# Kernel tuning notes

Measured on AMD Instinct MI355X. Metric: run time of the kernel, lower is better.

The kernel has to match this reference:

```python
import jax, jax.numpy as jnp
import numpy as np
import math

B, L, D, H, DFF = 2, 2048, 1024, 16, 4096

def _mha(xq, xkv, Wq, bq, Wk, bk, Wv, bv, Wo, bo, mask, h):
    # xq: [B,Lq,D], xkv: [B,Lk,D], mask: [B,1,Lq,Lk] bool
    b, lq, d = xq.shape
    dk = d // h
    q = (xq @ Wq + bq).reshape(b, lq, h, dk).transpose(0, 2, 1, 3)        # [B,h,Lq,dk]
    k = (xkv @ Wk + bk).reshape(b, -1, h, dk).transpose(0, 2, 1, 3)       # [B,h,Lk,dk]
    v = (xkv @ Wv + bv).reshape(b, -1, h, dk).transpose(0, 2, 1, 3)       # [B,h,Lk,dk]
    scores = jnp.einsum('bhqd,bhkd->bhqk', q, k) / jnp.sqrt(jnp.float32(dk))
    scores = jnp.where(mask, scores, jnp.float32(-1e9))                   # masked_fill(mask==0, -1e9)
    prob = jax.nn.softmax(scores, axis=-1)
    out = jnp.einsum('bhqk,bhkd->bhqd', prob, v)
    out = out.transpose(0, 2, 1, 3).reshape(b, lq, d)
    return out @ Wo + bo

def setup_inputs() -> dict:
    key = jax.random.key(0)
    ks = jax.random.split(key, 16)
    s = 0.02
    inp = {
        'tgt': jax.random.normal(ks[0], (B, L, D), jnp.float32),
        'encoder_out': jax.random.normal(ks[1], (B, L, D), jnp.float32),
        'tgt_mask': jnp.broadcast_to(jnp.tril(jnp.ones((L, L), bool)), (B, 1, L, L)),
        'src_tgt_mask': jnp.ones((B, 1, L, L), bool),
    }
    names = ['sWq','sWk','sWv','sWo','cWq','cWk','cWv','cWo']
    for i, n in enumerate(names):
        inp[n] = s * jax.random.normal(ks[2 + i], (D, D), jnp.float32)
        inp['sb' + n[2] if n[0] == 's' else 'cb' + n[2]] = jnp.zeros((D,), jnp.float32)
    inp['W1'] = s * jax.random.normal(ks[10], (D, DFF), jnp.float32)
    inp['b1'] = jnp.zeros((DFF,), jnp.float32)
    inp['W2'] = s * jax.random.normal(ks[11], (DFF, D), jnp.float32)
    inp['b2'] = jnp.zeros((D,), jnp.float32)
    return inp

def reference(tgt, encoder_out, tgt_mask, src_tgt_mask,
              sWq, sbq, sWk, sbk, sWv, sbv, sWo, sbo,
              cWq, cbq, cWk, cbk, cWv, cbv, cWo, cbo,
              W1, b1, W2, b2):
    # residual 1: masked self-attention (no norm)
    x = tgt + _mha(tgt, tgt, sWq, sbq, sWk, sbk, sWv, sbv, sWo, sbo, tgt_mask, H)
    # residual 2: cross-attention over encoder_out
    x = x + _mha(x, encoder_out, cWq, cbq, cWk, cbk, cWv, cbv, cWo, cbo, src_tgt_mask, H)
    # residual 3: position-wise FFN with ReLU
    x = x + (jax.nn.relu(x @ W1 + b1) @ W2 + b2)
    return x
```

## Files before the change

kernel.cpp:

```cpp
#include <hip/hip_runtime.h>

typedef unsigned short u16;
typedef unsigned int u32;
typedef __attribute__((ext_vector_type(8))) short short8;
typedef __attribute__((ext_vector_type(8))) __bf16 bf16x8;
typedef __attribute__((ext_vector_type(4))) float f32x4;
typedef __attribute__((ext_vector_type(4))) u16 u16x4;
typedef __attribute__((ext_vector_type(2))) u32 u32x2;

#define GLD16(gp, lp) __builtin_amdgcn_global_load_lds( \
    (const __attribute__((address_space(1))) unsigned int*)(gp), \
    (__attribute__((address_space(3))) unsigned int*)(lp), 16, 0, 0)

#if defined(__has_builtin) && __has_builtin(__builtin_amdgcn_exp2f)
#define EXP2(x) __builtin_amdgcn_exp2f(x)
#else
static __device__ __forceinline__ float exp2_asm(float x){
  float r; asm("v_exp_f32 %0, %1" : "=v"(r) : "v"(x)); return r;
}
#define EXP2(x) exp2_asm(x)
#endif

__device__ __forceinline__ float bf2f(u16 u){
  unsigned x = ((unsigned)u) << 16; float f; __builtin_memcpy(&f, &x, 4); return f;
}
__device__ __forceinline__ u16 f2bf(float f){
  unsigned x; __builtin_memcpy(&x, &f, 4);
  x += 0x7fffu + ((x >> 16) & 1u);
  return (u16)(x >> 16);
}
__device__ __forceinline__ u32 pkhi(float lo, float hi){
  u32 a, b; __builtin_memcpy(&a, &lo, 4); __builtin_memcpy(&b, &hi, 4);
  return __builtin_amdgcn_perm(b, a, 0x07060302u);
}
__device__ __forceinline__ f32x4 mfma_bf16(short8 a, short8 b, f32x4 c){
  return __builtin_amdgcn_mfma_f32_16x16x32_bf16(
      __builtin_bit_cast(bf16x8, a), __builtin_bit_cast(bf16x8, b), c, 0, 0, 0);
}

__global__ __launch_bounds__(256) void k_conv(const float* __restrict__ s, u16* __restrict__ d, int n){
  int i4 = (blockIdx.x * 256 + threadIdx.x) * 4;
  if (i4 < n){
    float4 v = *(const float4*)(s + i4);
    u16x4 o; o.x = f2bf(v.x); o.y = f2bf(v.y); o.z = f2bf(v.z); o.w = f2bf(v.w);
    *(u16x4*)(d + i4) = o;
  }
}

__global__ __launch_bounds__(256) void k_transpose(const float* __restrict__ s, u16* __restrict__ d, int K, int N){
  __shared__ float t[32][33];
  int bx = blockIdx.x * 32, by = blockIdx.y * 32;
  int x = threadIdx.x & 31, y = threadIdx.x >> 5;
  #pragma unroll
  for (int i = 0; i < 4; i++)
    t[y + i*8][x] = s[(size_t)(by + y + i*8) * N + bx + x];
  __syncthreads();
  #pragma unroll
  for (int i = 0; i < 4; i++)
    d[(size_t)(bx + y + i*8) * K + by + x] = f2bf(t[x][y + i*8]);
}

struct TP8 { const float* s[8]; u16* d[8]; };
__global__ __launch_bounds__(256) void k_transpose8(TP8 p){
  __shared__ float t[32][33];
  const float* s = p.s[blockIdx.z];
  u16* d = p.d[blockIdx.z];
  int bx = blockIdx.x * 32, by = blockIdx.y * 32;
  int x = threadIdx.x & 31, y = threadIdx.x >> 5;
  #pragma unroll
  for (int i = 0; i < 4; i++)
    t[y + i*8][x] = s[(size_t)(by + y + i*8) * 1024 + bx + x];
  __syncthreads();
  #pragma unroll
  for (int i = 0; i < 4; i++)
    d[(size_t)(bx + y + i*8) * 1024 + by + x] = f2bf(t[x][y + i*8]);
}

__global__ __launch_bounds__(256) void k_packbias(
    const float* __restrict__ sbq, const float* __restrict__ sbk,
    const float* __restrict__ sbv, const float* __restrict__ cbk,
    const float* __restrict__ cbv, float* __restrict__ pbS,
    float* __restrict__ pbC){
  int i = blockIdx.x * 256 + threadIdx.x;
  if (i < 3072) pbS[i] = (i < 1024) ? sbq[i] : (i < 2048 ? sbk[i-1024] : sbv[i-2048]);
  if (i < 2048) pbC[i] = (i < 1024) ? cbk[i] : cbv[i-1024];
}

template<int EPI, int BM, int BN, int KU>
__global__ __launch_bounds__(256, 2) void k_gemm_bt(
    const u16* __restrict__ A, const u16* __restrict__ BT,
    const float* __restrict__ bias, const float* __restrict__ resid,
    float* __restrict__ outF, u16* __restrict__ outB,
    int M, int N, int K, int vt_start, u16* __restrict__ Vt){
  constexpr int MI = BM / 32, NI = BN / 32;
  __shared__ u16 As[2*KU][BM*32];
  __shared__ u16 Bs[2*KU][BN*32];
  int tid = threadIdx.x, wave = tid >> 6, lane = tid & 63;
  int bm = blockIdx.x * BM, bn = blockIdx.y * BN;
  int wm = (wave & 1) * (BM/2), wn = (wave >> 1) * (BN/2);
  int l15 = lane & 15, quad = lane >> 4;

  f32x4 z = {0.f, 0.f, 0.f, 0.f};
  f32x4 acc[MI][NI];
  #pragma unroll
  for (int a = 0; a < MI; a++)
    #pragma unroll
    for (int b = 0; b < NI; b++) acc[a][b] = z;

  int sr = wave*16 + (lane >> 2);
  int sc = (lane & 3) * 8;
  const u16* Ag = A  + (size_t)(bm + sr) * K + sc;
  const u16* Bg = BT + (size_t)(bn + sr) * K + sc;
  int NKP = (K >> 5) / KU;

  #pragma unroll
  for (int u = 0; u < KU; u++){
    #pragma unroll
    for (int i = 0; i < BM/64; i++)
      GLD16(Ag + (size_t)(i*64)*K + u*32, &As[u][(wave*16 + i*64) * 32]);
    #pragma unroll
    for (int i = 0; i < BN/64; i++)
      GLD16(Bg + (size_t)(i*64)*K + u*32, &Bs[u][(wave*16 + i*64) * 32]);
  }

  for (int kt = 0; kt < NKP; kt++){
    __syncthreads();
    int cur = (kt & 1) * KU;
    if (kt + 1 < NKP){
      int nb = cur ^ KU;
      #pragma unroll
      for (int u = 0; u < KU; u++){
        int k0 = ((kt + 1) * KU + u) * 32;
        #pragma unroll
        for (int i = 0; i < BM/64; i++)
          GLD16(Ag + (size_t)(i*64)*K + k0, &As[nb+u][(wave*16 + i*64) * 32]);
        #pragma unroll
        for (int i = 0; i < BN/64; i++)
          GLD16(Bg + (size_t)(i*64)*K + k0, &Bs[nb+u][(wave*16 + i*64) * 32]);
      }
    }
    #pragma unroll
    for (int u = 0; u < KU; u++){
      short8 af[MI], bf[NI];
      #pragma unroll
      for (int mi = 0; mi < MI; mi++)
        af[mi] = *(const short8*)&As[cur+u][(wm + mi*16 + l15)*32 + quad*8];
      #pragma unroll
      for (int ni = 0; ni < NI; ni++)
        bf[ni] = *(const short8*)&Bs[cur+u][(wn + ni*16 + l15)*32 + quad*8];
      #pragma unroll
      for (int mi = 0; mi < MI; mi++)
        #pragma unroll
        for (int ni = 0; ni < NI; ni++)
          acc[mi][ni] = mfma_bf16(af[mi], bf[ni], acc[mi][ni]);
    }
  }

  #pragma unroll
  for (int mi = 0; mi < MI; mi++){
    #pragma unroll
    for (int ni = 0; ni < NI; ni++){
      int col = bn + wn + ni*16 + l15;
      float bv = bias[col];
      if (EPI == 0 && col >= vt_start){
        int vc = col - vt_start;
        int hh = vc >> 6, dd = vc & 63;
        int row0 = bm + wm + mi*16 + quad*4;
        int bb = row0 >> 11, ll = row0 & 2047;
        u16x4 vv;
        #pragma unroll
        for (int r = 0; r < 4; r++) vv[r] = f2bf(acc[mi][ni][r] + bv);
        *(u16x4*)&Vt[(((size_t)bb*16 + hh)*64 + dd)*2048 + ll] = vv;
      } else {
        #pragma unroll
        for (int r = 0; r < 4; r++){
          int row = bm + wm + mi*16 + quad*4 + r;
          float v = acc[mi][ni][r] + bv;
          if (EPI == 1) v = v > 0.f ? v : 0.f;
          size_t idx = (size_t)row * N + col;
          if (EPI >= 2) v += resid[idx];
          if (EPI == 2 || EPI == 3) outF[idx] = v;
          if (EPI != 3) outB[idx] = f2bf(v);
        }
      }
    }
  }
}

template<bool CAUSAL>
__global__ __launch_bounds__(256, 2) void k_flash(
    const u16* __restrict__ Q, int ldq,
    const u16* __restrict__ Kg, int ldk,
    const u16* __restrict__ Vt,
    u16* __restrict__ O, int ldo){
  __shared__ u16 Ks[128*64];
  __shared__ u16 Vs[64*128];
  __shared__ u16 Ps[128*128];
  int tid = threadIdx.x, wave = tid >> 6, lane = tid & 63;
  int l15 = lane & 15, quad = lane >> 4;
  int bx = blockIdx.x;
  int qt = CAUSAL ? ((bx & 1) ? (15 - (bx >> 1)) : (bx >> 1)) : bx;
  int bh = blockIdx.y;
  int b = bh >> 4, h = bh & 15;
  size_t bL = (size_t)b * 2048;
  const u16* qp = Q  + (bL + qt*128) * (size_t)ldq + h*64;
  const u16* kp = Kg + bL * (size_t)ldk + h*64;
  const u16* vtp = Vt + (size_t)bh * 64 * 2048;
  int wm = wave * 32;

  const float QSCALE = 0.125f * 1.44269504088896f;
  short8 qf[2][2];
  #pragma unroll
  for (int mi = 0; mi < 2; mi++)
    #pragma unroll
    for (int ks = 0; ks < 2; ks++){
      short8 t = *(const short8*)(qp + (size_t)(wm + mi*16 + l15)*ldq + ks*32 + quad*8);
      #pragma unroll
      for (int j = 0; j < 8; j++)
        t[j] = (short)f2bf(bf2f((u16)t[j]) * QSCALE);
      qf[mi][ks] = t;
    }

  f32x4 z = {0.f, 0.f, 0.f, 0.f};
  f32x4 o[2][4];
  float mrow[2], lrow[2];
  #pragma unroll
  for (int mi = 0; mi < 2; mi++){ mrow[mi] = -3.0e38f; lrow[mi] = 0.f; }
  #pragma unroll
  for (int mi = 0; mi < 2; mi++)
    #pragma unroll
    for (int nd = 0; nd < 4; nd++) o[mi][nd] = z;

  int nkt = CAUSAL ? (qt + 1) : 16;
  for (int kt = 0; kt < nkt; kt++){
    int cg = ((lane & 7) ^ ((lane >> 3) & 7)) * 8;
    #pragma unroll
    for (int i = 0; i < 4; i++){
      int r = i*32 + wave*8 + (lane >> 3);
      GLD16(kp + (size_t)(kt*128 + r) * ldk + cg, &Ks[(i*32 + wave*8) * 64]);
    }
    #pragma unroll
    for (int i = 0; i < 4; i++){
      int d0 = i*16 + wave*4;
      int d = d0 + (lane >> 4);
      int j = lane & 15;
      int chunk = (j & 8) | ((j ^ (d & 7)) & 7);
      GLD16(vtp + (size_t)d*2048 + kt*128 + chunk*8, &Vs[d0*128]);
    }
    __syncthreads();

    f32x4 s[2][8];
    #pragma unroll
    for (int mi = 0; mi < 2; mi++)
      #pragma unroll
      for (int nk = 0; nk < 8; nk++) s[mi][nk] = z;
    #pragma unroll
    for (int ks = 0; ks < 2; ks++){
      short8 kf[8];
      #pragma unroll
      for (int nk = 0; nk < 8; nk++){
        int row = nk*16 + l15;
        kf[nk] = *(const short8*)&Ks[row*64 + (((ks*4 + quad) ^ (row & 7)))*8];
      }
      #pragma unroll
      for (int mi = 0; mi < 2; mi++)
        #pragma unroll
        for (int nk = 0; nk < 8; nk++)
          s[mi][nk] = mfma_bf16(kf[nk], qf[mi][ks], s[mi][nk]);
    }

    if (CAUSAL && kt == qt){
      #pragma unroll
      for (int mi = 0; mi < 2; mi++){
        int q = wm + mi*16 + l15;
        #pragma unroll
        for (int nk = 0; nk < 8; nk++)
          #pragma unroll
          for (int r = 0; r < 4; r++){
            int key = nk*16 + quad*4 + r;
            if (key > q) s[mi][nk][r] = -1e30f;
          }
      }
    }

    #pragma unroll
    for (int mi = 0; mi < 2; mi++){
      float mx = s[mi][0][0];
      #pragma unroll
      for (int nk = 0; nk < 8; nk++)
        #pragma unroll
        for (int r = 0; r < 4; r++) mx = fmaxf(mx, s[mi][nk][r]);
      mx = fmaxf(mx, __shfl_xor(mx, 16));
      mx = fmaxf(mx, __shfl_xor(mx, 32));
      float mnew = fmaxf(mrow[mi], mx);
      float alpha = EXP2(mrow[mi] - mnew);
      mrow[mi] = mnew;
      float ls = 0.f;
      #pragma unroll
      for (int nk = 0; nk < 8; nk++)
        #pragma unroll
        for (int r = 0; r < 4; r++){
          float p = EXP2(s[mi][nk][r] - mnew);
          s[mi][nk][r] = p;
          ls += p;
        }
      ls += __shfl_xor(ls, 16);
      ls += __shfl_xor(ls, 32);
      lrow[mi] = lrow[mi] * alpha + ls;
      #pragma unroll
      for (int r = 0; r < 4; r++){
        float ar = __shfl(alpha, quad*20 + r);
        #pragma unroll
        for (int nd = 0; nd < 4; nd++) o[mi][nd][r] *= ar;
      }
    }

    #pragma unroll
    for (int mi = 0; mi < 2; mi++){
      int row = wm + mi*16 + l15;
      #pragma unroll
      for (int nk = 0; nk < 8; nk++){
        u32x2 pw;
        pw.x = pkhi(s[mi][nk][0], s[mi][nk][1]);
        pw.y = pkhi(s[mi][nk][2], s[mi][nk][3]);
        int c = nk*4 + quad;
        int phys = c ^ (row & 14);
        *(u32x2*)&Ps[row*128 + phys*4] = pw;
      }
    }

    #pragma unroll
    for (int kc = 0; kc < 4; kc++){
      short8 vf[4], pf[2];
      #pragma unroll
      for (int nd = 0; nd < 4; nd++){
        int d = nd*16 + l15;
        int cc = kc*4 + quad;
        int phys = (cc & 8) | ((cc ^ (d & 7)) & 7);
        vf[nd] = *(const short8*)&Vs[d*128 + phys*8];
      }
      #pragma unroll
      for (int mi = 0; mi < 2; mi++){
        int row = wm + mi*16 + l15;
        int c = kc*8 + quad*2;
        int phys = c ^ (row & 14);
        pf[mi] = *(const short8*)&Ps[row*128 + phys*4];
      }
      #pragma unroll
      for (int mi = 0; mi < 2; mi++)
        #pragma unroll
        for (int nd = 0; nd < 4; nd++)
          o[mi][nd] = mfma_bf16(pf[mi], vf[nd], o[mi][nd]);
    }
    __syncthreads();
  }

  u16* op = O + (bL + qt*128) * (size_t)ldo + h*64;
  #pragma unroll
  for (int mi = 0; mi < 2; mi++){
    float invl = 1.f / lrow[mi];
    #pragma unroll
    for (int r = 0; r < 4; r++){
      float ir = __shfl(invl, quad*20 + r);
      #pragma unroll
      for (int nd = 0; nd < 4; nd++)
        op[(size_t)(wm + mi*16 + quad*4 + r)*ldo + nd*16 + l15] = f2bf(o[mi][nd][r] * ir);
    }
  }
}

extern "C" void kernel_launch(void* const* d_in, const int* in_sizes, int n_in,
                              void* d_out, int out_size, void* d_ws, size_t ws_size,
                              hipStream_t stream){
  (void)in_sizes; (void)n_in; (void)out_size; (void)ws_size;
  const float* tgt = (const float*)d_in[0];
  const float* enc = (const float*)d_in[1];
  const float* sWq = (const float*)d_in[4];  const float* sbq = (const float*)d_in[5];
  const float* sWk = (const float*)d_in[6];  const float* sbk = (const float*)d_in[7];
  const float* sWv = (const float*)d_in[8];  const float* sbv = (const float*)d_in[9];
  const float* sWo = (const float*)d_in[10]; const float* sbo = (const float*)d_in[11];
  const float* cWq = (const float*)d_in[12]; const float* cbq = (const float*)d_in[13];
  const float* cWk = (const float*)d_in[14]; const float* cbk = (const float*)d_in[15];
  const float* cWv = (const float*)d_in[16]; const float* cbv = (const float*)d_in[17];
  const float* cWo = (const float*)d_in[18]; const float* cbo = (const float*)d_in[19];
  const float* W1  = (const float*)d_in[20]; const float* b1  = (const float*)d_in[21];
  const float* W2  = (const float*)d_in[22]; const float* b2  = (const float*)d_in[23];
  float* out = (float*)d_out;

  const int M = 4096;
  const int NEVER = 1 << 30;
  char* w = (char*)d_ws;
  auto alloc = [&](size_t bytes)->void*{ void* p = w; w += (bytes + 255) & ~(size_t)255; return p; };
  u16* tb    = (u16*)alloc((size_t)M*1024*2);
  u16* eb    = (u16*)alloc((size_t)M*1024*2);
  u16* qkv   = (u16*)alloc((size_t)M*3072*2);
  u16* ao    = (u16*)alloc((size_t)M*1024*2);
  u16* xb    = (u16*)alloc((size_t)M*1024*2);
  float* x1f = (float*)alloc((size_t)M*1024*4);
  u16* hbuf  = (u16*)alloc((size_t)M*4096*2);
  u16* VtS   = (u16*)alloc((size_t)32*64*2048*2);
  u16* VtC   = (u16*)alloc((size_t)32*64*2048*2);
  u16* sQKVT = (u16*)alloc((size_t)3072*1024*2);
  u16* sWoT  = (u16*)alloc((size_t)1024*1024*2);
  u16* cWqT  = (u16*)alloc((size_t)1024*1024*2);
  u16* cKVT  = (u16*)alloc((size_t)2048*1024*2);
  u16* cWoT  = (u16*)alloc((size_t)1024*1024*2);
  u16* W1T   = (u16*)alloc((size_t)4096*1024*2);
  u16* W2T   = (u16*)alloc((size_t)1024*4096*2);
  float* pbS = (float*)alloc(3072*4);
  float* pbC = (float*)alloc(2048*4);
  u16* cq  = tb;
  u16* ckv = qkv;

  k_conv<<<dim3(4096), 256, 0, stream>>>(tgt, tb, M*1024);
  k_conv<<<dim3(4096), 256, 0, stream>>>(enc, eb, M*1024);
  TP8 tp;
  tp.s[0]=sWq; tp.s[1]=sWk; tp.s[2]=sWv; tp.s[3]=sWo;
  tp.s[4]=cWq; tp.s[5]=cWk; tp.s[6]=cWv; tp.s[7]=cWo;
  tp.d[0]=sQKVT; tp.d[1]=sQKVT+1024*1024; tp.d[2]=sQKVT+2048*1024; tp.d[3]=sWoT;
  tp.d[4]=cWqT; tp.d[5]=cKVT; tp.d[6]=cKVT+1024*1024; tp.d[7]=cWoT;
  k_transpose8<<<dim3(32,32,8), 256, 0, stream>>>(tp);
  k_transpose<<<dim3(128,32), 256, 0, stream>>>(W1, W1T, 1024, 4096);
  k_transpose<<<dim3(32,128), 256, 0, stream>>>(W2, W2T, 4096, 1024);
  k_packbias<<<dim3(12), 256, 0, stream>>>(sbq, sbk, sbv, cbk, cbv, pbS, pbC);

  k_gemm_bt<0,128,128,1><<<dim3(32,24), 256, 0, stream>>>(tb, sQKVT, pbS, nullptr, nullptr, qkv, M, 3072, 1024, 2048, VtS);
  k_flash<true><<<dim3(16,32), 256, 0, stream>>>(qkv, 3072, qkv+1024, 3072, VtS, ao, 1024);
  k_gemm_bt<2,64,64,2><<<dim3(64,16), 256, 0, stream>>>(ao, sWoT, sbo, tgt, x1f, xb, M, 1024, 1024, NEVER, nullptr);

  k_gemm_bt<0,64,64,2><<<dim3(64,16), 256, 0, stream>>>(xb, cWqT, cbq, nullptr, nullptr, cq, M, 1024, 1024, NEVER, nullptr);
  k_gemm_bt<0,128,128,1><<<dim3(32,16), 256, 0, stream>>>(eb, cKVT, pbC, nullptr, nullptr, ckv, M, 2048, 1024, 1024, VtC);
  k_flash<false><<<dim3(16,32), 256, 0, stream>>>(cq, 1024, ckv, 2048, VtC, ao, 1024);
  k_gemm_bt<2,64,64,2><<<dim3(64,16), 256, 0, stream>>>(ao, cWoT, cbo, x1f, x1f, xb, M, 1024, 1024, NEVER, nullptr);

  k_gemm_bt<1,128,128,1><<<dim3(32,32), 256, 0, stream>>>(xb, W1T, b1, nullptr, nullptr, hbuf, M, 4096, 1024, NEVER, nullptr);
  k_gemm_bt<3,64,64,2><<<dim3(64,16), 256, 0, stream>>>(hbuf, W2T, b2, x1f, out, nullptr, M, 1024, 4096, NEVER, nullptr);
}
```

Baseline: 543.4 us.

## Shrink flash tiles to 64x64 and double-buffer K/V loads in LDS

The flash attention kernel now handles 64 query rows per block with 64-key tiles instead of 128x128. K and V tiles are double-buffered in LDS, so the next tile's global-to-LDS load is issued while the current tile is computed. The smaller tiles double the grid, cut LDS use and registers, and raise the launch bound to 4 blocks per CU for more occupancy and better causal load balance. The cost is half the MFMA work per wave for each K/V load, more loop iterations and more barriers.

```diff
diff --git a/kernel.cpp b/kernel.cpp
--- a/kernel.cpp
+++ b/kernel.cpp
@@ -188,184 +188,166 @@
 }
 
 template<bool CAUSAL>
-__global__ __launch_bounds__(256, 2) void k_flash(
+__global__ __launch_bounds__(256, 4) void k_flash(
     const u16* __restrict__ Q, int ldq,
     const u16* __restrict__ Kg, int ldk,
     const u16* __restrict__ Vt,
     u16* __restrict__ O, int ldo){
-  __shared__ u16 Ks[128*64];
-  __shared__ u16 Vs[64*128];
-  __shared__ u16 Ps[128*128];
+  __shared__ u16 Ks[2][64*64];
+  __shared__ u16 Vs[2][64*64];
+  __shared__ u16 Ps[64*64];
   int tid = threadIdx.x, wave = tid >> 6, lane = tid & 63;
   int l15 = lane & 15, quad = lane >> 4;
   int bx = blockIdx.x;
-  int qt = CAUSAL ? ((bx & 1) ? (15 - (bx >> 1)) : (bx >> 1)) : bx;
+  int qt = CAUSAL ? ((bx & 1) ? (31 - (bx >> 1)) : (bx >> 1)) : bx;
   int bh = blockIdx.y;
   int b = bh >> 4, h = bh & 15;
   size_t bL = (size_t)b * 2048;
-  const u16* qp = Q  + (bL + qt*128) * (size_t)ldq + h*64;
+  const u16* qp = Q  + (bL + qt*64) * (size_t)ldq + h*64;
   const u16* kp = Kg + bL * (size_t)ldk + h*64;
   const u16* vtp = Vt + (size_t)bh * 64 * 2048;
-  int wm = wave * 32;
+  int wm = wave * 16;
 
   const float QSCALE = 0.125f * 1.44269504088896f;
-  short8 qf[2][2];
-  #pragma unroll
-  for (int mi = 0; mi < 2; mi++)
+  short8 qf[2];
+  #pragma unroll
+  for (int ks = 0; ks < 2; ks++){
+    short8 t = *(const short8*)(qp + (size_t)(wm + l15)*ldq + ks*32 + quad*8);
+    #pragma unroll
+    for (int j = 0; j < 8; j++)
+      t[j] = (short)f2bf(bf2f((u16)t[j]) * QSCALE);
+    qf[ks] = t;
+  }
+
+  f32x4 z = {0.f, 0.f, 0.f, 0.f};
+  f32x4 o[4];
+  float mrow = -3.0e38f, lrow = 0.f;
+  #pragma unroll
+  for (int nd = 0; nd < 4; nd++) o[nd] = z;
+
+  int srow = wave*8 + (lane >> 3);
+  int scol = ((lane & 7) ^ ((lane >> 3) & 7)) * 8;
+
+  int nkt = CAUSAL ? (qt + 1) : 32;
+  #pragma unroll
+  for (int i = 0; i < 2; i++)
+    GLD16(kp + (size_t)(i*32 + srow) * ldk + scol, &Ks[0][(i*32 + wave*8) * 64]);
+  #pragma unroll
+  for (int i = 0; i < 2; i++)
+    GLD16(vtp + (size_t)(i*32 + srow) * 2048 + scol, &Vs[0][(i*32 + wave*8) * 64]);
+
+  for (int kt = 0; kt < nkt; kt++){
+    __syncthreads();
+    int cur = kt & 1;
+    if (kt + 1 < nkt){
+      int nb = cur ^ 1;
+      #pragma unroll
+      for (int i = 0; i < 2; i++)
+        GLD16(kp + (size_t)((kt+1)*64 + i*32 + srow) * ldk + scol, &Ks[nb][(i*32 + wave*8) * 64]);
+      #pragma unroll
+      for (int i = 0; i < 2; i++)
+        GLD16(vtp + (size_t)(i*32 + srow) * 2048 + (kt+1)*64 + scol, &Vs[nb][(i*32 + wave*8) * 64]);
+    }
+
+    f32x4 s[4];
+    #pragma unroll
+    for (int nk = 0; nk < 4; nk++) s[nk] = z;
     #pragma unroll
     for (int ks = 0; ks < 2; ks++){
-      short8 t = *(const short8*)(qp + (size_t)(wm + mi*16 + l15)*ldq + ks*32 + quad*8);
-      #pragma unroll
-      for (int j = 0; j < 8; j++)
-        t[j] = (short)f2bf(bf2f((u16)t[j]) * QSCALE);
-      qf[mi][ks] = t;
-    }
-
-  f32x4 z = {0.f, 0.f, 0.f, 0.f};
-  f32x4 o[2][4];
-  float mrow[2], lrow[2];
-  #pragma unroll
-  for (int mi = 0; mi < 2; mi++){ mrow[mi] = -3.0e38f; lrow[mi] = 0.f; }
-  #pragma unroll
-  for (int mi = 0; mi < 2; mi++)
-    #pragma unroll
-    for (int nd = 0; nd < 4; nd++) o[mi][nd] = z;
-
-  int nkt = CAUSAL ? (qt + 1) : 16;
-  for (int kt = 0; kt < nkt; kt++){
-    int cg = ((lane & 7) ^ ((lane >> 3) & 7)) * 8;
-    #pragma unroll
-    for (int i = 0; i < 4; i++){
-      int r = i*32 + wave*8 + (lane >> 3);
-      GLD16(kp + (size_t)(kt*128 + r) * ldk + cg, &Ks[(i*32 + wave*8) * 64]);
-    }
-    #pragma unroll
-    for (int i = 0; i < 4; i++){
-      int d0 = i*16 + wave*4;
-      int d = d0 + (lane >> 4);
-      int j = lane & 15;
-      int chunk = (j & 8) | ((j ^ (d & 7)) & 7);
-      GLD16(vtp + (size_t)d*2048 + kt*128 + chunk*8, &Vs[d0*128]);
-    }
-    __syncthreads();
-
-    f32x4 s[2][8];
-    #pragma unroll
-    for (int mi = 0; mi < 2; mi++)
-      #pragma unroll
-      for (int nk = 0; nk < 8; nk++) s[mi][nk] = z;
-    #pragma unroll
-    for (int ks = 0; ks < 2; ks++){
-      short8 kf[8];
-      #pragma unroll
-      for (int nk = 0; nk < 8; nk++){
+      short8 kf[4];
+      #pragma unroll
+      for (int nk = 0; nk < 4; nk++){
         int row = nk*16 + l15;
-        kf[nk] = *(const short8*)&Ks[row*64 + (((ks*4 + quad) ^ (row & 7)))*8];
-      }
-      #pragma unroll
-      for (int mi = 0; mi < 2; mi++)
-        #pragma unroll
-        for (int nk = 0; nk < 8; nk++)
-          s[mi][nk] = mfma_bf16(kf[nk], qf[mi][ks], s[mi][nk]);
+        kf[nk] = *(const short8*)&Ks[cur][row*64 + (((ks*4 + quad) ^ (row & 7)))*8];
+      }
+      #pragma unroll
+      for (int nk = 0; nk < 4; nk++)
+        s[nk] = mfma_bf16(kf[nk], qf[ks], s[nk]);
     }
 
     if (CAUSAL && kt == qt){
-      #pragma unroll
-      for (int mi = 0; mi < 2; mi++){
-        int q = wm + mi*16 + l15;
-        #pragma unroll
-        for (int nk = 0; nk < 8; nk++)
-          #pragma unroll
-          for (int r = 0; r < 4; r++){
-            int key = nk*16 + quad*4 + r;
-            if (key > q) s[mi][nk][r] = -1e30f;
-          }
-      }
-    }
-
-    #pragma unroll
-    for (int mi = 0; mi < 2; mi++){
-      float mx = s[mi][0][0];
-      #pragma unroll
-      for (int nk = 0; nk < 8; nk++)
-        #pragma unroll
-        for (int r = 0; r < 4; r++) mx = fmaxf(mx, s[mi][nk][r]);
+      int q = wm + l15;
+      #pragma unroll
+      for (int nk = 0; nk < 4; nk++)
+        #pragma unroll
+        for (int r = 0; r < 4; r++){
+          int key = nk*16 + quad*4 + r;
+          if (key > q) s[nk][r] = -1e30f;
+        }
+    }
+
+    {
+      float mx = s[0][0];
+      #pragma unroll
+      for (int nk = 0; nk < 4; nk++)
+        #pragma unroll
+        for (int r = 0; r < 4; r++) mx = fmaxf(mx, s[nk][r]);
       mx = fmaxf(mx, __shfl_xor(mx, 16));
       mx = fmaxf(mx, __shfl_xor(mx, 32));
-      float mnew = fmaxf(mrow[mi], mx);
-      float alpha = EXP2(mrow[mi] - mnew);
-      mrow[mi] = mnew;
+      float mnew = fmaxf(mrow, mx);
+      float alpha = EXP2(mrow - mnew);
+      mrow = mnew;
       float ls = 0.f;
       #pragma unroll
-      for (int nk = 0; nk < 8; nk++)
+      for (int nk = 0; nk < 4; nk++)
         #pragma unroll
         for (int r = 0; r < 4; r++){
-          float p = EXP2(s[mi][nk][r] - mnew);
-          s[mi][nk][r] = p;
+          float p = EXP2(s[nk][r] - mnew);
+          s[nk][r] = p;
           ls += p;
         }
       ls += __shfl_xor(ls, 16);
       ls += __shfl_xor(ls, 32);
-      lrow[mi] = lrow[mi] * alpha + ls;
+      lrow = lrow * alpha + ls;
       #pragma unroll
       for (int r = 0; r < 4; r++){
         float ar = __shfl(alpha, quad*20 + r);
         #pragma unroll
-        for (int nd = 0; nd < 4; nd++) o[mi][nd][r] *= ar;
-      }
-    }
-
-    #pragma unroll
-    for (int mi = 0; mi < 2; mi++){
-      int row = wm + mi*16 + l15;
-      #pragma unroll
-      for (int nk = 0; nk < 8; nk++){
+        for (int nd = 0; nd < 4; nd++) o[nd][r] *= ar;
+      }
+    }
+
+    {
+      int row = wm + l15;
+      #pragma unroll
+      for (int nk = 0; nk < 4; nk++){
         u32x2 pw;
-        pw.x = pkhi(s[mi][nk][0], s[mi][nk][1]);
-        pw.y = pkhi(s[mi][nk][2], s[mi][nk][3]);
+        pw.x = pkhi(s[nk][0], s[nk][1]);
+        pw.y = pkhi(s[nk][2], s[nk][3]);
         int c = nk*4 + quad;
         int phys = c ^ (row & 14);
-        *(u32x2*)&Ps[row*128 + phys*4] = pw;
-      }
-    }
-
-    #pragma unroll
-    for (int kc = 0; kc < 4; kc++){
-      short8 vf[4], pf[2];
+        *(u32x2*)&Ps[row*64 + phys*4] = pw;
+      }
+    }
+
+    #pragma unroll
+    for (int kc = 0; kc < 2; kc++){
+      short8 vf[4];
       #pragma unroll
       for (int nd = 0; nd < 4; nd++){
         int d = nd*16 + l15;
         int cc = kc*4 + quad;
-        int phys = (cc & 8) | ((cc ^ (d & 7)) & 7);
-        vf[nd] = *(const short8*)&Vs[d*128 + phys*8];
-      }
-      #pragma unroll
-      for (int mi = 0; mi < 2; mi++){
-        int row = wm + mi*16 + l15;
-        int c = kc*8 + quad*2;
-        int phys = c ^ (row & 14);
-        pf[mi] = *(const short8*)&Ps[row*128 + phys*4];
-      }
-      #pragma unroll
-      for (int mi = 0; mi < 2; mi++)
-        #pragma unroll
-        for (int nd = 0; nd < 4; nd++)
-          o[mi][nd] = mfma_bf16(pf[mi], vf[nd], o[mi][nd]);
-    }
-    __syncthreads();
-  }
-
-  u16* op = O + (bL + qt*128) * (size_t)ldo + h*64;
-  #pragma unroll
-  for (int mi = 0; mi < 2; mi++){
-    float invl = 1.f / lrow[mi];
-    #pragma unroll
-    for (int r = 0; r < 4; r++){
-      float ir = __shfl(invl, quad*20 + r);
+        int phys = cc ^ (d & 7);
+        vf[nd] = *(const short8*)&Vs[cur][d*64 + phys*8];
+      }
+      int row = wm + l15;
+      int pc = kc*8 + quad*2;
+      int pphys = pc ^ (row & 14);
+      short8 pf = *(const short8*)&Ps[row*64 + pphys*4];
       #pragma unroll
       for (int nd = 0; nd < 4; nd++)
-        op[(size_t)(wm + mi*16 + quad*4 + r)*ldo + nd*16 + l15] = f2bf(o[mi][nd][r] * ir);
-    }
+        o[nd] = mfma_bf16(pf, vf[nd], o[nd]);
+    }
+  }
+
+  u16* op = O + (bL + qt*64) * (size_t)ldo + h*64;
+  float invl = 1.f / lrow;
+  #pragma unroll
+  for (int r = 0; r < 4; r++){
+    float ir = __shfl(invl, quad*20 + r);
+    #pragma unroll
+    for (int nd = 0; nd < 4; nd++)
+      op[(size_t)(wm + quad*4 + r)*ldo + nd*16 + l15] = f2bf(o[nd][r] * ir);
   }
 }
 
@@ -425,12 +407,12 @@
   k_packbias<<<dim3(12), 256, 0, stream>>>(sbq, sbk, sbv, cbk, cbv, pbS, pbC);
 
   k_gemm_bt<0,128,128,1><<<dim3(32,24), 256, 0, stream>>>(tb, sQKVT, pbS, nullptr, nullptr, qkv, M, 3072, 1024, 2048, VtS);
-  k_flash<true><<<dim3(16,32), 256, 0, stream>>>(qkv, 3072, qkv+1024, 3072, VtS, ao, 1024);
+  k_flash<true><<<dim3(32,32), 256, 0, stream>>>(qkv, 3072, qkv+1024, 3072, VtS, ao, 1024);
   k_gemm_bt<2,64,64,2><<<dim3(64,16), 256, 0, stream>>>(ao, sWoT, sbo, tgt, x1f, xb, M, 1024, 1024, NEVER, nullptr);
 
   k_gemm_bt<0,64,64,2><<<dim3(64,16), 256, 0, stream>>>(xb, cWqT, cbq, nullptr, nullptr, cq, M, 1024, 1024, NEVER, nullptr);
   k_gemm_bt<0,128,128,1><<<dim3(32,16), 256, 0, stream>>>(eb, cKVT, pbC, nullptr, nullptr, ckv, M, 2048, 1024, 1024, VtC);
-  k_flash<false><<<dim3(16,32), 256, 0, stream>>>(cq, 1024, ckv, 2048, VtC, ao, 1024);
+  k_flash<false><<<dim3(32,32), 256, 0, stream>>>(cq, 1024, ckv, 2048, VtC, ao, 1024);
   k_gemm_bt<2,64,64,2><<<dim3(64,16), 256, 0, stream>>>(ao, cWoT, cbo, x1f, x1f, xb, M, 1024, 1024, NEVER, nullptr);
 
   k_gemm_bt<1,128,128,1><<<dim3(32,32), 256, 0, stream>>>(xb, W1T, b1, nullptr, nullptr, hbuf, M, 4096, 1024, NEVER, nullptr);
```

Result: slower. 555.8 us (+2.3%).

## Double-buffer K/V tiles in flash attention and add lazy softmax rescaling

Applied to the files above, without the earlier changes.

The flash-attention kernel now keeps two LDS buffers each for K and V. It loads the first tile before the loop and prefetches tile kt+1 while computing on tile kt, so global-to-LDS latency can hide behind MFMA work. One barrier per iteration replaces two. The online-softmax rescale of the output and row sum is skipped unless some row's max grows by more than 8 in log2 units, which saves exp and multiply work. The P staging buffer is halved by writing and consuming P in two half-tiles per wave. Total LDS per block grows, so fitting two blocks per CU now depends on the per-CU LDS capacity.

```diff
diff --git a/kernel.cpp b/kernel.cpp
--- a/kernel.cpp
+++ b/kernel.cpp
@@ -193,9 +193,9 @@
     const u16* __restrict__ Kg, int ldk,
     const u16* __restrict__ Vt,
     u16* __restrict__ O, int ldo){
-  __shared__ u16 Ks[128*64];
-  __shared__ u16 Vs[64*128];
-  __shared__ u16 Ps[128*128];
+  __shared__ u16 Ks[2][128*64];
+  __shared__ u16 Vs[2][64*128];
+  __shared__ u16 Ps[128*64];
   int tid = threadIdx.x, wave = tid >> 6, lane = tid & 63;
   int l15 = lane & 15, quad = lane >> 4;
   int bx = blockIdx.x;
@@ -232,22 +232,40 @@
     for (int nd = 0; nd < 4; nd++) o[mi][nd] = z;
 
   int nkt = CAUSAL ? (qt + 1) : 16;
+  int cg = ((lane & 7) ^ ((lane >> 3) & 7)) * 8;
+  #pragma unroll
+  for (int i = 0; i < 4; i++){
+    int r = i*32 + wave*8 + (lane >> 3);
+    GLD16(kp + (size_t)r * ldk + cg, &Ks[0][(i*32 + wave*8) * 64]);
+  }
+  #pragma unroll
+  for (int i = 0; i < 4; i++){
+    int d0 = i*16 + wave*4;
+    int d = d0 + (lane >> 4);
+    int j = lane & 15;
+    int chunk = (j & 8) | ((j ^ (d & 7)) & 7);
+    GLD16(vtp + (size_t)d*2048 + chunk*8, &Vs[0][d0*128]);
+  }
+
   for (int kt = 0; kt < nkt; kt++){
-    int cg = ((lane & 7) ^ ((lane >> 3) & 7)) * 8;
-    #pragma unroll
-    for (int i = 0; i < 4; i++){
-      int r = i*32 + wave*8 + (lane >> 3);
-      GLD16(kp + (size_t)(kt*128 + r) * ldk + cg, &Ks[(i*32 + wave*8) * 64]);
-    }
-    #pragma unroll
-    for (int i = 0; i < 4; i++){
-      int d0 = i*16 + wave*4;
-      int d = d0 + (lane >> 4);
-      int j = lane & 15;
-      int chunk = (j & 8) | ((j ^ (d & 7)) & 7);
-      GLD16(vtp + (size_t)d*2048 + kt*128 + chunk*8, &Vs[d0*128]);
-    }
     __syncthreads();
+    int cur = kt & 1;
+    if (kt + 1 < nkt){
+      int nb = cur ^ 1;
+      #pragma unroll
+      for (int i = 0; i < 4; i++){
+        int r = i*32 + wave*8 + (lane >> 3);
+        GLD16(kp + (size_t)((kt+1)*128 + r) * ldk + cg, &Ks[nb][(i*32 + wave*8) * 64]);
+      }
+      #pragma unroll
+      for (int i = 0; i < 4; i++){
+        int d0 = i*16 + wave*4;
+        int d = d0 + (lane >> 4);
+        int j = lane & 15;
+        int chunk = (j & 8) | ((j ^ (d & 7)) & 7);
+        GLD16(vtp + (size_t)d*2048 + (kt+1)*128 + chunk*8, &Vs[nb][d0*128]);
+      }
+    }
 
     f32x4 s[2][8];
     #pragma unroll
@@ -260,7 +278,7 @@
       #pragma unroll
       for (int nk = 0; nk < 8; nk++){
         int row = nk*16 + l15;
-        kf[nk] = *(const short8*)&Ks[row*64 + (((ks*4 + quad) ^ (row & 7)))*8];
+        kf[nk] = *(const short8*)&Ks[cur][row*64 + (((ks*4 + quad) ^ (row & 7)))*8];
       }
       #pragma unroll
       for (int mi = 0; mi < 2; mi++)
@@ -292,67 +310,73 @@
         for (int r = 0; r < 4; r++) mx = fmaxf(mx, s[mi][nk][r]);
       mx = fmaxf(mx, __shfl_xor(mx, 16));
       mx = fmaxf(mx, __shfl_xor(mx, 32));
-      float mnew = fmaxf(mrow[mi], mx);
-      float alpha = EXP2(mrow[mi] - mnew);
-      mrow[mi] = mnew;
+      if (!__all(mx - mrow[mi] <= 8.f)){
+        float mnew = fmaxf(mrow[mi], mx);
+        float alpha = EXP2(mrow[mi] - mnew);
+        mrow[mi] = mnew;
+        lrow[mi] *= alpha;
+        #pragma unroll
+        for (int r = 0; r < 4; r++){
+          float ar = __shfl(alpha, quad*20 + r);
+          #pragma unroll
+          for (int nd = 0; nd < 4; nd++) o[mi][nd][r] *= ar;
+        }
+      }
       float ls = 0.f;
       #pragma unroll
       for (int nk = 0; nk < 8; nk++)
         #pragma unroll
         for (int r = 0; r < 4; r++){
-          float p = EXP2(s[mi][nk][r] - mnew);
+          float p = EXP2(s[mi][nk][r] - mrow[mi]);
           s[mi][nk][r] = p;
           ls += p;
         }
       ls += __shfl_xor(ls, 16);
       ls += __shfl_xor(ls, 32);
-      lrow[mi] = lrow[mi] * alpha + ls;
-      #pragma unroll
-      for (int r = 0; r < 4; r++){
-        float ar = __shfl(alpha, quad*20 + r);
-        #pragma unroll
-        for (int nd = 0; nd < 4; nd++) o[mi][nd][r] *= ar;
-      }
-    }
-
-    #pragma unroll
-    for (int mi = 0; mi < 2; mi++){
-      int row = wm + mi*16 + l15;
-      #pragma unroll
-      for (int nk = 0; nk < 8; nk++){
-        u32x2 pw;
-        pw.x = pkhi(s[mi][nk][0], s[mi][nk][1]);
-        pw.y = pkhi(s[mi][nk][2], s[mi][nk][3]);
-        int c = nk*4 + quad;
-        int phys = c ^ (row & 14);
-        *(u32x2*)&Ps[row*128 + phys*4] = pw;
-      }
-    }
-
-    #pragma unroll
-    for (int kc = 0; kc < 4; kc++){
-      short8 vf[4], pf[2];
-      #pragma unroll
-      for (int nd = 0; nd < 4; nd++){
-        int d = nd*16 + l15;
-        int cc = kc*4 + quad;
-        int phys = (cc & 8) | ((cc ^ (d & 7)) & 7);
-        vf[nd] = *(const short8*)&Vs[d*128 + phys*8];
-      }
+      lrow[mi] += ls;
+    }
+
+    #pragma unroll
+    for (int half = 0; half < 2; half++){
       #pragma unroll
       for (int mi = 0; mi < 2; mi++){
         int row = wm + mi*16 + l15;
-        int c = kc*8 + quad*2;
-        int phys = c ^ (row & 14);
-        pf[mi] = *(const short8*)&Ps[row*128 + phys*4];
-      }
-      #pragma unroll
-      for (int mi = 0; mi < 2; mi++)
-        #pragma unroll
-        for (int nd = 0; nd < 4; nd++)
-          o[mi][nd] = mfma_bf16(pf[mi], vf[nd], o[mi][nd]);
-    }
-    __syncthreads();
+        #pragma unroll
+        for (int nkl = 0; nkl < 4; nkl++){
+          int nk = half*4 + nkl;
+          u32x2 pw;
+          pw.x = pkhi(s[mi][nk][0], s[mi][nk][1]);
+          pw.y = pkhi(s[mi][nk][2], s[mi][nk][3]);
+          int c = nkl*4 + quad;
+          int phys = c ^ (row & 14);
+          *(u32x2*)&Ps[row*64 + phys*4] = pw;
+        }
+      }
+      #pragma unroll
+      for (int kcl = 0; kcl < 2; kcl++){
+        int kc = half*2 + kcl;
+        short8 vf[4], pf[2];
+        #pragma unroll
+        for (int nd = 0; nd < 4; nd++){
+          int d = nd*16 + l15;
+          int cc = kc*4 + quad;
+          int phys = (cc & 8) | ((cc ^ (d & 7)) & 7);
+          vf[nd] = *(const short8*)&Vs[cur][d*128 + phys*8];
+        }
+        #pragma unroll
+        for (int mi = 0; mi < 2; mi++){
+          int row = wm + mi*16 + l15;
+          int pc = kcl*8 + quad*2;
+          int pphys = pc ^ (row & 14);
+          pf[mi] = *(const short8*)&Ps[row*64 + pphys*4];
+        }
+        #pragma unroll
+        for (int mi = 0; mi < 2; mi++)
+          #pragma unroll
+          for (int nd = 0; nd < 4; nd++)
+            o[mi][nd] = mfma_bf16(pf[mi], vf[nd], o[mi][nd]);
+      }
+    }
   }
 
   u16* op = O + (bL + qt*128) * (size_t)ldo + h*64;
```

Measured after the change: 536.0 us. Within noise of the previous version (-1.4%).
